# Optimization experiments

Hardware: AMD Instinct MI355X
Metric: run time of the kernel (lower is better)

Reference implementation:

```python
import jax, jax.numpy as jnp
import numpy as np

D_HIDDEN = 1024
N_HEAD = 16
D_HEAD = D_HIDDEN // N_HEAD  # 64
B, F = 4, 2048


def setup_inputs() -> dict:
    key = jax.random.key(0)
    ks = jax.random.split(key, 10)
    std = 0.02
    inp = {
        "q": jax.random.normal(ks[0], (B, F, D_HIDDEN), jnp.float32),
        "k": jax.random.normal(ks[1], (B, F, D_HIDDEN), jnp.float32),
        "v": jax.random.normal(ks[2], (B, F, D_HIDDEN), jnp.float32),
        # additive mask: 1 = masked position (scaled by -1e9 inside); all-zero = no masking
        "attention_mask": jnp.zeros((B, F, F), jnp.float32),
        # Dense layer params (Keras Dense: y = x @ W + b)
        "qw_w": jax.random.truncated_normal(ks[3], -2, 2, (D_HIDDEN, D_HIDDEN), jnp.float32) * std,
        "qw_b": jnp.zeros((D_HIDDEN,), jnp.float32),
        "kw_w": jax.random.truncated_normal(ks[4], -2, 2, (D_HIDDEN, D_HIDDEN), jnp.float32) * std,
        "kw_b": jnp.zeros((D_HIDDEN,), jnp.float32),
        "vw_w": jax.random.truncated_normal(ks[5], -2, 2, (D_HIDDEN, D_HIDDEN), jnp.float32) * std,
        "vw_b": jnp.zeros((D_HIDDEN,), jnp.float32),
        # output projection kernel (n_head, d_head, d_hidden)
        "out_kernel": jax.random.truncated_normal(ks[6], -2, 2, (N_HEAD, D_HEAD, D_HIDDEN), jnp.float32) * std,
    }
    return inp


def reference(q, k, v, attention_mask, qw_w, qw_b, kw_w, kw_b, vw_w, vw_b, out_kernel):
    b, f, _ = q.shape
    # linear projections
    qh = q @ qw_w + qw_b
    kh = k @ kw_w + kw_b
    vh = v @ vw_w + vw_b
    # split heads: [B, F, H, D] -> [B, H, F, D]
    def split(x):
        return x.reshape(b, -1, N_HEAD, D_HEAD).transpose(0, 2, 1, 3)
    qh, kh, vh = split(qh), split(kh), split(vh)
    # scaled dot-product attention with additive mask (1 -> -1e9)
    scores = jnp.einsum('BNFD,BNfD->BNFf', qh, kh) / jnp.sqrt(jnp.asarray(D_HEAD, qh.dtype))
    scores = scores + attention_mask[:, None, :, :] * jnp.asarray(-1e9, scores.dtype)
    probs = jax.nn.softmax(scores, axis=-1)
    out = jnp.einsum('BNFf,BNfD->BNFD', probs, vh)
    out = out.transpose(0, 2, 1, 3)  # BNFD -> BFND
    return jnp.einsum('BFND,NDM->BFM', out, out_kernel)
```

## Files before the change

### kernel.cpp

```cpp
#include <hip/hip_runtime.h>


typedef unsigned short u16;
typedef __attribute__((ext_vector_type(8))) short short8;
typedef __attribute__((ext_vector_type(4))) float f32x4;
typedef __attribute__((ext_vector_type(16))) float f32x16;

#define SC2 0.18033688011112042f
#define MSC -1.4426950408889634e9f
#define THR 8.0f

__device__ __forceinline__ u16 f2bf(float x) {
  unsigned int u = __float_as_uint(x);
  u += 0x7FFFu + ((u >> 16) & 1u);
  return (u16)(u >> 16);
}

__device__ __forceinline__ void gload16(const void* g, void* l) {
  __builtin_amdgcn_global_load_lds(
      (const __attribute__((address_space(1))) void*)g,
      (__attribute__((address_space(3))) void*)l, 16, 0, 0);
}

__device__ __forceinline__ uint4 pack8(const u16* t) {
  uint4 o;
  o.x = (unsigned)t[0] | ((unsigned)t[1] << 16);
  o.y = (unsigned)t[2] | ((unsigned)t[3] << 16);
  o.z = (unsigned)t[4] | ((unsigned)t[5] << 16);
  o.w = (unsigned)t[6] | ((unsigned)t[7] << 16);
  return o;
}

__device__ __forceinline__ unsigned cvtpk(float lo, float hi) {
  unsigned r;
  asm("v_cvt_pk_bf16_f32 %0, %1, %2" : "=v"(r) : "v"(lo), "v"(hi));
  return r;
}

__global__ __launch_bounds__(256) void masksum(const float* __restrict__ mask,
                                               unsigned char* __restrict__ msum) {
  int t = blockIdx.x * 256 + threadIdx.x;
  int row = t & 2047;
  int kt = (t >> 11) & 31;
  int b = t >> 16;
  const float4* p =
      (const float4*)(mask + ((size_t)(b * 2048 + row)) * 2048 + kt * 64);
  unsigned acc = 0;
#pragma unroll
  for (int i = 0; i < 16; i++) {
    float4 f = p[i];
    acc |= __float_as_uint(f.x) | __float_as_uint(f.y) |
           __float_as_uint(f.z) | __float_as_uint(f.w);
  }
  msum[t] = acc ? 1 : 0;
}

__global__ __launch_bounds__(256) void wtrans(
    const float* __restrict__ w0, const float* __restrict__ w1,
    const float* __restrict__ w2, const float* __restrict__ w3,
    u16* __restrict__ o0, u16* __restrict__ o1,
    u16* __restrict__ o2, u16* __restrict__ o3) {
  const float* W; u16* O;
  switch (blockIdx.z) {
    case 0: W = w0; O = o0; break;
    case 1: W = w1; O = o1; break;
    case 2: W = w2; O = o2; break;
    default: W = w3; O = o3; break;
  }
  __shared__ u16 T[64][72];
  const int t = threadIdx.x, r = t >> 2, seg = t & 3;
  const int k0 = blockIdx.y * 64, n0 = blockIdx.x * 64;
  const float* src = W + (size_t)(k0 + r) * 1024 + n0 + seg * 16;
#pragma unroll
  for (int jj = 0; jj < 4; jj++) {
    float4 f = ((const float4*)src)[jj];
    T[r][seg * 16 + jj * 4 + 0] = f2bf(f.x);
    T[r][seg * 16 + jj * 4 + 1] = f2bf(f.y);
    T[r][seg * 16 + jj * 4 + 2] = f2bf(f.z);
    T[r][seg * 16 + jj * 4 + 3] = f2bf(f.w);
  }
  __syncthreads();
  u16 tmp[16];
#pragma unroll
  for (int j = 0; j < 16; j++) tmp[j] = T[seg * 16 + j][r];
  u16* dst = O + (size_t)(n0 + r) * 1024 + k0 + seg * 16;
  ((uint4*)dst)[0] = pack8(tmp);
  ((uint4*)dst)[1] = pack8(tmp + 8);
}

__global__ __launch_bounds__(256) void gemm_proj3(
    const float* __restrict__ Aq, const float* __restrict__ Ak,
    const float* __restrict__ Av, const u16* __restrict__ Wq,
    const u16* __restrict__ Wk, const u16* __restrict__ Wv,
    const float* __restrict__ bq, const float* __restrict__ bk,
    const float* __restrict__ bv, u16* __restrict__ oq,
    u16* __restrict__ ok, u16* __restrict__ ovT) {
  constexpr int K = 1024, N = 1024;
  __shared__ u16 sbuf[128 * 136];
  u16* lsA = sbuf;
  u16* lsB = sbuf + 128 * 32;
  const int z = blockIdx.z;
  const float* A = (z == 0) ? Aq : (z == 1) ? Ak : Av;
  const u16* Bt = (z == 0) ? Wq : (z == 1) ? Wk : Wv;
  const float* bias = (z == 0) ? bq : (z == 1) ? bk : bv;

  const int tid = threadIdx.x;
  const int w = tid >> 6, lane = tid & 63;
  const int l15 = lane & 15, lg = lane >> 4;
  const int fid = blockIdx.x + (blockIdx.y << 3);
  const int virt = ((fid & 7) << 6) + (fid >> 3);
  const int m0 = (virt >> 3) << 7, n0 = (virt & 7) << 7;
  const int wr = w >> 1, wc = w & 1;

  f32x4 acc[4][4];
#pragma unroll
  for (int i = 0; i < 4; i++)
#pragma unroll
    for (int j = 0; j < 4; j++) acc[i][j] = f32x4{0.f, 0.f, 0.f, 0.f};

  const float* As = A + (size_t)(m0 + w * 32 + (lane >> 2)) * K + (lane & 3) * 8;
  const u16* Bs = Bt + (size_t)(n0 + w * 32 + (lane >> 2)) * K + (lane & 3) * 8;
  u16* lB = &lsB[(w * 32) * 32];
  u16* lAw = &lsA[(w * 32 + (lane >> 2)) * 32 + (lane & 3) * 8];

  float4 a0 = *(const float4*)(As);
  float4 a1 = *(const float4*)(As + 4);
  float4 a2 = *(const float4*)(As + 16 * K);
  float4 a3 = *(const float4*)(As + 16 * K + 4);

  for (int k0 = 0; k0 < K; k0 += 32) {
    gload16(Bs + k0, lB);
    gload16(Bs + 16 * K + k0, lB + 16 * 32);
    uint4 pa, pb;
    pa.x = cvtpk(a0.x, a0.y); pa.y = cvtpk(a0.z, a0.w);
    pa.z = cvtpk(a1.x, a1.y); pa.w = cvtpk(a1.z, a1.w);
    pb.x = cvtpk(a2.x, a2.y); pb.y = cvtpk(a2.z, a2.w);
    pb.z = cvtpk(a3.x, a3.y); pb.w = cvtpk(a3.z, a3.w);
    *(uint4*)lAw = pa;
    *(uint4*)(lAw + 16 * 32) = pb;
    if (k0 + 32 < K) {
      a0 = *(const float4*)(As + k0 + 32);
      a1 = *(const float4*)(As + k0 + 36);
      a2 = *(const float4*)(As + 16 * K + k0 + 32);
      a3 = *(const float4*)(As + 16 * K + k0 + 36);
    }
    __syncthreads();
    short8 af[4], bfv[4];
#pragma unroll
    for (int mi = 0; mi < 4; mi++)
      af[mi] = *(const short8*)&lsA[(wr * 64 + mi * 16 + l15) * 32 + lg * 8];
#pragma unroll
    for (int nj = 0; nj < 4; nj++)
      bfv[nj] = *(const short8*)&lsB[(wc * 64 + nj * 16 + l15) * 32 + lg * 8];
#pragma unroll
    for (int mi = 0; mi < 4; mi++)
#pragma unroll
      for (int nj = 0; nj < 4; nj++)
        acc[mi][nj] = __builtin_amdgcn_mfma_f32_16x16x32_bf16(af[mi], bfv[nj],
                                                              acc[mi][nj], 0, 0, 0);
    __syncthreads();
  }

  const int crow = m0 + wr * 64 + lg * 4;
  const int ccol = n0 + wc * 64 + l15;
  if (z < 2) {
    u16* C = (z == 0) ? oq : ok;
    const float scl = (z == 0) ? SC2 : 1.0f;
#pragma unroll
    for (int nj = 0; nj < 4; nj++) {
      float bv = bias[ccol + nj * 16];
#pragma unroll
      for (int mi = 0; mi < 4; mi++)
#pragma unroll
        for (int r = 0; r < 4; r++)
          C[(size_t)(crow + mi * 16 + r) * N + ccol + nj * 16] =
              f2bf((acc[mi][nj][r] + bv) * scl);
    }
  } else {
    const int rl = wr * 64 + lg * 4;
    const int cl = wc * 64 + l15;
#pragma unroll
    for (int nj = 0; nj < 4; nj++) {
      float bv = bias[ccol + nj * 16];
#pragma unroll
      for (int mi = 0; mi < 4; mi++)
#pragma unroll
        for (int r = 0; r < 4; r++)
          sbuf[(rl + mi * 16 + r) * 136 + cl + nj * 16] =
              f2bf(acc[mi][nj][r] + bv);
    }
    __syncthreads();
    const int drow = tid >> 1, seg = tid & 1;
    const int b = m0 >> 11;
    const int f0 = (m0 & 2047) + seg * 64;
    u16* dst = ovT + (size_t)(b * 1024 + n0 + drow) * 2048 + f0;
#pragma unroll
    for (int c = 0; c < 8; c++) {
      u16 tmp[8];
#pragma unroll
      for (int j = 0; j < 8; j++)
        tmp[j] = sbuf[(seg * 64 + c * 8 + j) * 136 + drow];
      ((uint4*)dst)[c] = pack8(tmp);
    }
  }
}

__global__ __launch_bounds__(256) void gemm_out(
    const u16* __restrict__ A, const u16* __restrict__ Bt,
    float* __restrict__ C) {
  constexpr int K = 1024, N = 1024;
  __shared__ u16 lsA[128 * 32];
  __shared__ u16 lsB[128 * 32];
  const int tid = threadIdx.x;
  const int w = tid >> 6, lane = tid & 63;
  const int l15 = lane & 15, lg = lane >> 4;
  const int m0 = blockIdx.y << 7, n0 = blockIdx.x << 7;
  const int wr = w >> 1, wc = w & 1;

  f32x4 acc[4][4];
#pragma unroll
  for (int i = 0; i < 4; i++)
#pragma unroll
    for (int j = 0; j < 4; j++) acc[i][j] = f32x4{0.f, 0.f, 0.f, 0.f};

  const u16* As = A + (size_t)(m0 + w * 32 + (lane >> 2)) * K + (lane & 3) * 8;
  const u16* Bs = Bt + (size_t)(n0 + w * 32 + (lane >> 2)) * K + (lane & 3) * 8;
  u16* lA = &lsA[(w * 32) * 32];
  u16* lB = &lsB[(w * 32) * 32];

  for (int k0 = 0; k0 < K; k0 += 32) {
    gload16(As + k0, lA);
    gload16(As + 16 * K + k0, lA + 16 * 32);
    gload16(Bs + k0, lB);
    gload16(Bs + 16 * K + k0, lB + 16 * 32);
    __syncthreads();
    short8 af[4], bfv[4];
#pragma unroll
    for (int mi = 0; mi < 4; mi++)
      af[mi] = *(const short8*)&lsA[(wr * 64 + mi * 16 + l15) * 32 + lg * 8];
#pragma unroll
    for (int nj = 0; nj < 4; nj++)
      bfv[nj] = *(const short8*)&lsB[(wc * 64 + nj * 16 + l15) * 32 + lg * 8];
#pragma unroll
    for (int mi = 0; mi < 4; mi++)
#pragma unroll
      for (int nj = 0; nj < 4; nj++)
        acc[mi][nj] = __builtin_amdgcn_mfma_f32_16x16x32_bf16(af[mi], bfv[nj],
                                                              acc[mi][nj], 0, 0, 0);
    __syncthreads();
  }

  const int crow = m0 + wr * 64 + lg * 4;
  const int ccol = n0 + wc * 64 + l15;
#pragma unroll
  for (int nj = 0; nj < 4; nj++)
#pragma unroll
    for (int mi = 0; mi < 4; mi++)
#pragma unroll
      for (int r = 0; r < 4; r++)
        C[(size_t)(crow + mi * 16 + r) * N + ccol + nj * 16] = acc[mi][nj][r];
}

__global__ __launch_bounds__(512, 4) void attn_fwd(
    const u16* __restrict__ qh, const u16* __restrict__ kh,
    const u16* __restrict__ vhT, const float* __restrict__ mask,
    const unsigned char* __restrict__ msum, u16* __restrict__ aout) {
  __shared__ u16 Kls[2][64][72];
  __shared__ u16 Vls[2][64][72];

  const int tid = threadIdx.x;
  const int w = tid >> 6, lane = tid & 63;
  const int l31 = lane & 31, hi = lane >> 5;
  const int blk = ((blockIdx.x & 7) << 6) | (blockIdx.x >> 3);
  const int qt = blk & 7, bh = blk >> 3, h = bh & 15, b = bh >> 4;
  const int frow = qt * 256 + w * 32;
  const size_t qrow0 = (size_t)b * 2048 + frow;

  short8 qf[4];
#pragma unroll
  for (int ds = 0; ds < 4; ds++)
    qf[ds] = *(const short8*)&qh[(qrow0 + l31) * 1024 + h * 64 + ds * 16 + hi * 8];

  f32x16 zf;
#pragma unroll
  for (int i = 0; i < 16; i++) zf[i] = 0.f;

  f32x16 oacc[2];
#pragma unroll
  for (int i = 0; i < 16; i++) { oacc[0][i] = 0.f; oacc[1][i] = 0.f; }
  float m_run = 0.f, l_run = 0.f;

  const int sr = tid >> 3, seg = tid & 7;
  const u16* Ksrc = kh + ((size_t)b * 2048 + sr) * 1024 + h * 64 + seg * 8;
  const u16* Vsrc = vhT + ((size_t)bh * 64 + sr) * 2048 + seg * 8;
  const unsigned char* msrow = msum + (size_t)b * 65536 + frow + l31;

  uint4 ka0, va0;
  unsigned char mb, mbn;
  {
    uint4 x0 = *(const uint4*)Ksrc;
    uint4 y0 = *(const uint4*)Vsrc;
    *(uint4*)&Kls[0][sr][seg * 8] = x0;
    *(uint4*)&Vls[0][sr][seg * 8] = y0;
    ka0 = *(const uint4*)(Ksrc + 64 * 1024);
    va0 = *(const uint4*)(Vsrc + 64);
    mb = msrow[0];
    mbn = msrow[2048];
  }
  __syncthreads();

  for (int kt = 0; kt < 32; kt++) {
    const int cur = kt & 1;
    const int k0 = kt * 64;
    const int mflag = __any((int)mb);
    mb = mbn;

    if (kt < 31) {
      *(uint4*)&Kls[cur ^ 1][sr][seg * 8] = ka0;
      *(uint4*)&Vls[cur ^ 1][sr][seg * 8] = va0;
    }
    if (kt < 30) {
      ka0 = *(const uint4*)(Ksrc + (size_t)(kt + 2) * 64 * 1024);
      va0 = *(const uint4*)(Vsrc + (kt + 2) * 64);
      mbn = msrow[(size_t)(kt + 2) * 2048];
    }

    f32x16 sacc[2];
#pragma unroll
    for (int kb = 0; kb < 2; kb++) {
      short8 kf[4];
#pragma unroll
      for (int ds = 0; ds < 4; ds++)
        kf[ds] = *(const short8*)&Kls[cur][kb * 32 + l31][ds * 16 + hi * 8];
      __builtin_amdgcn_s_setprio(1);
      sacc[kb] = __builtin_amdgcn_mfma_f32_32x32x16_bf16(kf[0], qf[0], zf, 0, 0, 0);
#pragma unroll
      for (int ds = 1; ds < 4; ds++)
        sacc[kb] = __builtin_amdgcn_mfma_f32_32x32x16_bf16(kf[ds], qf[ds],
                                                           sacc[kb], 0, 0, 0);
      __builtin_amdgcn_s_setprio(0);
    }

    if (mflag) {
      const size_t mrow = ((size_t)b * 2048 + frow + l31) * 2048 + (size_t)k0;
#pragma unroll
      for (int kb = 0; kb < 2; kb++)
#pragma unroll
        for (int r = 0; r < 16; r++) {
          float mv = mask[mrow + kb * 32 + (r & 3) + 8 * (r >> 2) + 4 * hi];
          sacc[kb][r] = fmaf(mv, MSC, sacc[kb][r]);
        }
      float mx[16];
#pragma unroll
      for (int r = 0; r < 16; r++) mx[r] = fmaxf(sacc[0][r], sacc[1][r]);
#pragma unroll
      for (int s = 8; s >= 1; s >>= 1)
#pragma unroll
        for (int r = 0; r < s; r++) mx[r] = fmaxf(mx[r], mx[r + s]);
      float tm = mx[0];
      tm = fmaxf(tm, __shfl_xor(tm, 32, 64));
      if (!__all(tm <= m_run + THR)) {
        float mnew = fmaxf(m_run, tm);
        float al = exp2f(m_run - mnew);
        m_run = mnew;
        l_run *= al;
#pragma unroll
        for (int r = 0; r < 16; r++) {
          float alr = __shfl(al, (r & 3) + 8 * (r >> 2) + 4 * hi, 64);
          oacc[0][r] *= alr;
          oacc[1][r] *= alr;
        }
      }
    }

    float rsp = 0.f, rsq = 0.f;
    unsigned pw[16];
    if (m_run == 0.f) {
#pragma unroll
      for (int kb = 0; kb < 2; kb++)
#pragma unroll
        for (int jp = 0; jp < 2; jp++) {
          float e[8];
#pragma unroll
          for (int t = 0; t < 8; t++)
            e[t] = exp2f(sacc[kb][8 * jp + t]);
          rsp += (e[0] + e[1]) + (e[2] + e[3]);
          rsq += (e[4] + e[5]) + (e[6] + e[7]);
          unsigned ye0 = cvtpk(e[0], e[1]);
          unsigned ye1 = cvtpk(e[2], e[3]);
          unsigned xo0 = cvtpk(e[4], e[5]);
          unsigned xo1 = cvtpk(e[6], e[7]);
          asm volatile("v_permlane32_swap_b32 %0, %1" : "+v"(ye0), "+v"(xo0));
          asm volatile("v_permlane32_swap_b32 %0, %1" : "+v"(ye1), "+v"(xo1));
          const int kk = kb * 2 + jp;
          pw[kk * 4 + 0] = ye0;
          pw[kk * 4 + 1] = ye1;
          pw[kk * 4 + 2] = xo0;
          pw[kk * 4 + 3] = xo1;
        }
    } else {
      const float mm = m_run;
#pragma unroll
      for (int kb = 0; kb < 2; kb++)
#pragma unroll
        for (int jp = 0; jp < 2; jp++) {
          float e[8];
#pragma unroll
          for (int t = 0; t < 8; t++)
            e[t] = exp2f(sacc[kb][8 * jp + t] - mm);
          rsp += (e[0] + e[1]) + (e[2] + e[3]);
          rsq += (e[4] + e[5]) + (e[6] + e[7]);
          unsigned ye0 = cvtpk(e[0], e[1]);
          unsigned ye1 = cvtpk(e[2], e[3]);
          unsigned xo0 = cvtpk(e[4], e[5]);
          unsigned xo1 = cvtpk(e[6], e[7]);
          asm volatile("v_permlane32_swap_b32 %0, %1" : "+v"(ye0), "+v"(xo0));
          asm volatile("v_permlane32_swap_b32 %0, %1" : "+v"(ye1), "+v"(xo1));
          const int kk = kb * 2 + jp;
          pw[kk * 4 + 0] = ye0;
          pw[kk * 4 + 1] = ye1;
          pw[kk * 4 + 2] = xo0;
          pw[kk * 4 + 3] = xo1;
        }
    }
    float rs = rsp + rsq;
    rs += __shfl_xor(rs, 32, 64);
    l_run += rs;

#pragma unroll
    for (int dn = 0; dn < 2; dn++) {
      short8 vf[4];
#pragma unroll
      for (int kk = 0; kk < 4; kk++)
        vf[kk] = *(const short8*)&Vls[cur][dn * 32 + l31][kk * 16 + hi * 8];
      __builtin_amdgcn_s_setprio(1);
#pragma unroll
      for (int kk = 0; kk < 4; kk++) {
        uint4 t4 = {pw[kk * 4 + 0], pw[kk * 4 + 1], pw[kk * 4 + 2], pw[kk * 4 + 3]};
        oacc[dn] = __builtin_amdgcn_mfma_f32_32x32x16_bf16(
            *(short8*)&t4, vf[kk], oacc[dn], 0, 0, 0);
      }
      __builtin_amdgcn_s_setprio(0);
    }

    __syncthreads();
  }

  float inv = 1.0f / l_run;
#pragma unroll
  for (int r = 0; r < 16; r++) {
    const int qr = (r & 3) + 8 * (r >> 2) + 4 * hi;
    float invr = __shfl(inv, qr, 64);
    aout[(qrow0 + qr) * 1024 + h * 64 + l31] = f2bf(oacc[0][r] * invr);
    aout[(qrow0 + qr) * 1024 + h * 64 + 32 + l31] = f2bf(oacc[1][r] * invr);
  }
}

extern "C" void kernel_launch(void* const* d_in, const int* in_sizes, int n_in,
                              void* d_out, int out_size, void* d_ws, size_t ws_size,
                              hipStream_t stream) {
  (void)in_sizes; (void)n_in; (void)out_size; (void)ws_size;
  const float* q    = (const float*)d_in[0];
  const float* k    = (const float*)d_in[1];
  const float* v    = (const float*)d_in[2];
  const float* mask = (const float*)d_in[3];
  const float* qw_w = (const float*)d_in[4];
  const float* qw_b = (const float*)d_in[5];
  const float* kw_w = (const float*)d_in[6];
  const float* kw_b = (const float*)d_in[7];
  const float* vw_w = (const float*)d_in[8];
  const float* vw_b = (const float*)d_in[9];
  const float* wo   = (const float*)d_in[10];

  u16* vhT = (u16*)d_ws;
  u16* qwT = vhT + 4096 * 2048;
  u16* kwT = qwT + 1024 * 1024;
  u16* vwT = kwT + 1024 * 1024;
  u16* woT = vwT + 1024 * 1024;
  u16* attn_o = woT + 1024 * 1024;
  unsigned char* msumb = (unsigned char*)(attn_o + 8192 * 1024);
  u16* qh = (u16*)d_out;
  u16* kh = qh + 8192 * 1024;

  wtrans<<<dim3(16, 16, 4), 256, 0, stream>>>(qw_w, kw_w, vw_w, wo,
                                              qwT, kwT, vwT, woT);
  gemm_proj3<<<dim3(8, 64, 3), 256, 0, stream>>>(q, k, v, qwT, kwT, vwT,
                                                 qw_b, kw_b, vw_b, qh, kh, vhT);
  masksum<<<1024, 256, 0, stream>>>(mask, msumb);
  attn_fwd<<<512, 512, 0, stream>>>(qh, kh, vhT, mask, msumb, attn_o);
  gemm_out<<<dim3(8, 64), 256, 0, stream>>>(attn_o, woT, (float*)d_out);
}
```

Before: 254.6 us.

## Double-buffer LDS tiles in QKV projection GEMM to overlap loads with MFMA

The projection GEMM main loop now alternates between two LDS buffers for the A and B tiles. The next tile's async global-to-LDS loads and the converted A stores are issued before the MFMA work on the current tile, so each k-step needs one barrier instead of two. The intent is to hide global and LDS load latency behind compute. In exchange, the GEMM's LDS footprint grows, although it still fits inside the existing shared buffer.

```diff
diff --git a/kernel.cpp b/kernel.cpp
--- a/kernel.cpp
+++ b/kernel.cpp
@@ -97,8 +97,6 @@
     u16* __restrict__ ok, u16* __restrict__ ovT) {
   constexpr int K = 1024, N = 1024;
   __shared__ u16 sbuf[128 * 136];
-  u16* lsA = sbuf;
-  u16* lsB = sbuf + 128 * 32;
   const int z = blockIdx.z;
   const float* A = (z == 0) ? Aq : (z == 1) ? Ak : Av;
   const u16* Bt = (z == 0) ? Wq : (z == 1) ? Wk : Wv;
@@ -120,38 +118,60 @@
 
   const float* As = A + (size_t)(m0 + w * 32 + (lane >> 2)) * K + (lane & 3) * 8;
   const u16* Bs = Bt + (size_t)(n0 + w * 32 + (lane >> 2)) * K + (lane & 3) * 8;
-  u16* lB = &lsB[(w * 32) * 32];
-  u16* lAw = &lsA[(w * 32 + (lane >> 2)) * 32 + (lane & 3) * 8];
+  const int lofs = w * 1024 + lane * 8;
 
   float4 a0 = *(const float4*)(As);
   float4 a1 = *(const float4*)(As + 4);
   float4 a2 = *(const float4*)(As + 16 * K);
   float4 a3 = *(const float4*)(As + 16 * K + 4);
-
-  for (int k0 = 0; k0 < K; k0 += 32) {
-    gload16(Bs + k0, lB);
-    gload16(Bs + 16 * K + k0, lB + 16 * 32);
+  gload16(Bs, sbuf + 8192 + w * 1024);
+  gload16(Bs + 16 * K, sbuf + 8192 + w * 1024 + 512);
+  {
     uint4 pa, pb;
     pa.x = cvtpk(a0.x, a0.y); pa.y = cvtpk(a0.z, a0.w);
     pa.z = cvtpk(a1.x, a1.y); pa.w = cvtpk(a1.z, a1.w);
     pb.x = cvtpk(a2.x, a2.y); pb.y = cvtpk(a2.z, a2.w);
     pb.z = cvtpk(a3.x, a3.y); pb.w = cvtpk(a3.z, a3.w);
-    *(uint4*)lAw = pa;
-    *(uint4*)(lAw + 16 * 32) = pb;
-    if (k0 + 32 < K) {
-      a0 = *(const float4*)(As + k0 + 32);
-      a1 = *(const float4*)(As + k0 + 36);
-      a2 = *(const float4*)(As + 16 * K + k0 + 32);
-      a3 = *(const float4*)(As + 16 * K + k0 + 36);
-    }
-    __syncthreads();
+    *(uint4*)(sbuf + lofs) = pa;
+    *(uint4*)(sbuf + lofs + 512) = pb;
+  }
+  a0 = *(const float4*)(As + 32);
+  a1 = *(const float4*)(As + 36);
+  a2 = *(const float4*)(As + 16 * K + 32);
+  a3 = *(const float4*)(As + 16 * K + 36);
+  __syncthreads();
+
+  for (int kt = 0; kt < 32; kt++) {
+    const int cur = kt & 1, nxt = cur ^ 1;
+    const int k0n = (kt + 1) * 32;
+    u16* lsAc = sbuf + cur * 4096;
+    u16* lsBc = sbuf + 8192 + cur * 4096;
+    if (kt < 31) {
+      u16* lsBn = sbuf + 8192 + nxt * 4096;
+      gload16(Bs + k0n, lsBn + w * 1024);
+      gload16(Bs + 16 * K + k0n, lsBn + w * 1024 + 512);
+      uint4 pa, pb;
+      pa.x = cvtpk(a0.x, a0.y); pa.y = cvtpk(a0.z, a0.w);
+      pa.z = cvtpk(a1.x, a1.y); pa.w = cvtpk(a1.z, a1.w);
+      pb.x = cvtpk(a2.x, a2.y); pb.y = cvtpk(a2.z, a2.w);
+      pb.z = cvtpk(a3.x, a3.y); pb.w = cvtpk(a3.z, a3.w);
+      u16* lsAn = sbuf + nxt * 4096;
+      *(uint4*)(lsAn + lofs) = pa;
+      *(uint4*)(lsAn + lofs + 512) = pb;
+      if (kt < 30) {
+        a0 = *(const float4*)(As + k0n + 32);
+        a1 = *(const float4*)(As + k0n + 36);
+        a2 = *(const float4*)(As + 16 * K + k0n + 32);
+        a3 = *(const float4*)(As + 16 * K + k0n + 36);
+      }
+    }
     short8 af[4], bfv[4];
 #pragma unroll
     for (int mi = 0; mi < 4; mi++)
-      af[mi] = *(const short8*)&lsA[(wr * 64 + mi * 16 + l15) * 32 + lg * 8];
+      af[mi] = *(const short8*)&lsAc[(wr * 64 + mi * 16 + l15) * 32 + lg * 8];
 #pragma unroll
     for (int nj = 0; nj < 4; nj++)
-      bfv[nj] = *(const short8*)&lsB[(wc * 64 + nj * 16 + l15) * 32 + lg * 8];
+      bfv[nj] = *(const short8*)&lsBc[(wc * 64 + nj * 16 + l15) * 32 + lg * 8];
 #pragma unroll
     for (int mi = 0; mi < 4; mi++)
 #pragma unroll
```

New measurement: 249.5 us, median of 3. 2.0% less time.
